# Kernel optimization log

Hardware: AMD Instinct MI355X
Metric: run time of the kernel (lower is better)

Reference implementation:

```python
import jax, jax.numpy as jnp
import numpy as np

KERN = 2  # matches init kwarg


def _avgpool(x):
    # non-overlapping avg pool kernel=stride=KERN on (N,C,H,W)
    N, C, H, W = x.shape
    return x.reshape(N, C, H // KERN, KERN, W // KERN, KERN).mean(axis=(3, 5))


def _pair_sum(mu1, var1, mu2, var2):
    # mu*, var*: (N, D). Broadcast to (N, N, D) and reduce to scalar.
    d = mu1[:, None, :] - mu2[None, :, :]
    s = var1[:, None, :] + var2[None, :, :]
    return jnp.sum(jnp.exp(-0.5 * (d * d / s + jnp.log(s))))


def setup_inputs() -> dict:
    key = jax.random.key(0)
    k1, k2, k3, k4 = jax.random.split(key, 4)
    shp = (128, 16, 32, 32)
    return {
        "mu_a": jax.random.normal(k1, shp, dtype=jnp.float32),
        "logvar_a": jax.random.normal(k2, shp, dtype=jnp.float32),
        "mu_b": jax.random.normal(k3, shp, dtype=jnp.float32),
        "logvar_b": jax.random.normal(k4, shp, dtype=jnp.float32),
    }


def reference(mu_a, logvar_a, mu_b, logvar_b):
    inv_k2 = 1.0 / (KERN * KERN)
    ma = _avgpool(mu_a)
    mb = _avgpool(mu_b)
    va = _avgpool(jnp.exp(logvar_a)) * inv_k2
    vb = _avgpool(jnp.exp(logvar_b)) * inv_k2
    N = ma.shape[0]
    ma, mb = ma.reshape(N, -1), mb.reshape(N, -1)
    va, vb = va.reshape(N, -1), vb.reshape(N, -1)
    vaa = _pair_sum(ma, va, ma, va)
    vab = _pair_sum(ma, va, mb, vb)
    vbb = _pair_sum(mb, vb, mb, vb)
    return vaa + vbb - 2.0 * vab
```

## Files before the change

kernel.cpp:

```cpp
#include <hip/hip_runtime.h>

#define NN 128
#define CC_ 16
#define HH 32
#define WW 32
#define DD 4096
#define ND (NN*DD)

#define MU_SCALE 0.8493218002880191f

__global__ __launch_bounds__(256) void pool_kernel(
    const float* __restrict__ mu_a, const float* __restrict__ lv_a,
    const float* __restrict__ mu_b, const float* __restrict__ lv_b,
    float* __restrict__ ws, float* __restrict__ out)
{
    int t = blockIdx.x * 256 + threadIdx.x;
    if (t == 0) out[0] = 0.0f;

    int wo = t & 15;
    int ho = (t >> 4) & 15;
    int c  = (t >> 8) & 15;
    int n  = t >> 12;

    int base = ((n * CC_ + c) * HH + 2 * ho) * WW + 2 * wo;

    float2 a0 = *(const float2*)(mu_a + base);
    float2 a1 = *(const float2*)(mu_a + base + WW);
    float2 la0 = *(const float2*)(lv_a + base);
    float2 la1 = *(const float2*)(lv_a + base + WW);
    float2 b0 = *(const float2*)(mu_b + base);
    float2 b1 = *(const float2*)(mu_b + base + WW);
    float2 lb0 = *(const float2*)(lv_b + base);
    float2 lb1 = *(const float2*)(lv_b + base + WW);

    const float ms = 0.25f * MU_SCALE;
    float ma_v = ms * (a0.x + a0.y + a1.x + a1.y);
    float mb_v = ms * (b0.x + b0.y + b1.x + b1.y);
    float va_v = 0.0625f * (__expf(la0.x) + __expf(la0.y) + __expf(la1.x) + __expf(la1.y));
    float vb_v = 0.0625f * (__expf(lb0.x) + __expf(lb0.y) + __expf(lb1.x) + __expf(lb1.y));

    ws[t]          = ma_v;
    ws[ND + t]     = va_v;
    ws[2 * ND + t] = mb_v;
    ws[3 * ND + t] = vb_v;
}

#define JCHUNK 32

__global__ __launch_bounds__(256) void pair_kernel(
    const float* __restrict__ ws, float* __restrict__ out)
{
    const float* __restrict__ ma = ws;
    const float* __restrict__ va = ws + ND;
    const float* __restrict__ mb = ws + 2 * ND;
    const float* __restrict__ vb = ws + 3 * ND;

    const int d  = blockIdx.x * 256 + threadIdx.x;
    const int i0 = (blockIdx.y >> 2) * 4;
    const int j0 = (blockIdx.y & 3) * JCHUNK;

    float rma[4], rva[4], rmb[4], rvb[4];
#pragma unroll
    for (int k = 0; k < 4; ++k) {
        rma[k] = ma[(i0 + k) * DD + d];
        rva[k] = va[(i0 + k) * DD + d];
        rmb[k] = mb[(i0 + k) * DD + d];
        rvb[k] = vb[(i0 + k) * DD + d];
    }

    float acc_aa = 0.0f, acc_bb = 0.0f, acc_ab = 0.0f;

    for (int j = j0; j < j0 + JCHUNK; ++j) {
        float jma = ma[j * DD + d];
        float jva = va[j * DD + d];
        float jmb = mb[j * DD + d];
        float jvb = vb[j * DD + d];
#pragma unroll
        for (int k = 0; k < 4; ++k) {
            {
                float dd = rma[k] - jma;
                float s  = rva[k] + jva;
                float r  = __builtin_amdgcn_rsqf(s);
                float q  = dd * r;
                float e  = __builtin_amdgcn_exp2f(-(q * q));
                acc_aa = fmaf(e, r, acc_aa);
            }
            {
                float dd = rmb[k] - jmb;
                float s  = rvb[k] + jvb;
                float r  = __builtin_amdgcn_rsqf(s);
                float q  = dd * r;
                float e  = __builtin_amdgcn_exp2f(-(q * q));
                acc_bb = fmaf(e, r, acc_bb);
            }
            {
                float dd = rma[k] - jmb;
                float s  = rva[k] + jvb;
                float r  = __builtin_amdgcn_rsqf(s);
                float q  = dd * r;
                float e  = __builtin_amdgcn_exp2f(-(q * q));
                acc_ab = fmaf(e, r, acc_ab);
            }
        }
    }

    float part = acc_aa + acc_bb - 2.0f * acc_ab;

#pragma unroll
    for (int off = 32; off > 0; off >>= 1)
        part += __shfl_down(part, off, 64);

    __shared__ float wsum[4];
    int lane = threadIdx.x & 63;
    int wv   = threadIdx.x >> 6;
    if (lane == 0) wsum[wv] = part;
    __syncthreads();
    if (threadIdx.x == 0) {
        float s = wsum[0] + wsum[1] + wsum[2] + wsum[3];
        atomicAdd(out, s);
    }
}

extern "C" void kernel_launch(void* const* d_in, const int* in_sizes, int n_in,
                              void* d_out, int out_size, void* d_ws, size_t ws_size,
                              hipStream_t stream) {
    const float* mu_a = (const float*)d_in[0];
    const float* lv_a = (const float*)d_in[1];
    const float* mu_b = (const float*)d_in[2];
    const float* lv_b = (const float*)d_in[3];
    float* out = (float*)d_out;
    float* ws  = (float*)d_ws;

    pool_kernel<<<dim3(ND / 256), 256, 0, stream>>>(mu_a, lv_a, mu_b, lv_b, ws, out);
    pair_kernel<<<dim3(DD / 256, (NN / 4) * (NN / JCHUNK)), 256, 0, stream>>>(ws, out);
}
```

Baseline: 134.0 us.

## Interleave pooled a/b buffers and use packed float2 math in pair kernel

The pool kernel now writes the a and b means as one float2 array and the a and b variances as another, so the pair kernel issues two 8-byte loads per j instead of four 4-byte loads. The pair kernel arithmetic moves to 2-wide vector types, meant to map subtract, add, multiply and fma onto packed FP32 instructions, and the j loop is unrolled by 2. rsq and exp2 stay scalar, and since the transcendentals likely bound the kernel, the gain may be limited.

After: 123.8 us. -7.6%, faster.

```diff
diff --git a/kernel.cpp b/kernel.cpp
--- a/kernel.cpp
+++ b/kernel.cpp
@@ -7,12 +7,14 @@
 #define DD 4096
 #define ND (NN*DD)
 
+typedef float v2f __attribute__((ext_vector_type(2)));
+
 #define MU_SCALE 0.8493218002880191f
 
 __global__ __launch_bounds__(256) void pool_kernel(
     const float* __restrict__ mu_a, const float* __restrict__ lv_a,
     const float* __restrict__ mu_b, const float* __restrict__ lv_b,
-    float* __restrict__ ws, float* __restrict__ out)
+    float2* __restrict__ wm, float2* __restrict__ wv, float* __restrict__ out)
 {
     int t = blockIdx.x * 256 + threadIdx.x;
     if (t == 0) out[0] = 0.0f;
@@ -39,72 +41,71 @@
     float va_v = 0.0625f * (__expf(la0.x) + __expf(la0.y) + __expf(la1.x) + __expf(la1.y));
     float vb_v = 0.0625f * (__expf(lb0.x) + __expf(lb0.y) + __expf(lb1.x) + __expf(lb1.y));
 
-    ws[t]          = ma_v;
-    ws[ND + t]     = va_v;
-    ws[2 * ND + t] = mb_v;
-    ws[3 * ND + t] = vb_v;
+    wm[t] = make_float2(ma_v, mb_v);
+    wv[t] = make_float2(va_v, vb_v);
 }
 
 #define JCHUNK 32
 
+__device__ __forceinline__ void pair_group(
+    v2f& acc, v2f mi, v2f mj, v2f vi, v2f vj)
+{
+    v2f dd = mi - mj;
+    v2f s  = vi + vj;
+    v2f r;
+    r.x = __builtin_amdgcn_rsqf(s.x);
+    r.y = __builtin_amdgcn_rsqf(s.y);
+    v2f q  = dd * r;
+    v2f qq = q * q;
+    v2f e;
+    e.x = __builtin_amdgcn_exp2f(-qq.x);
+    e.y = __builtin_amdgcn_exp2f(-qq.y);
+    acc += e * r;
+}
+
 __global__ __launch_bounds__(256) void pair_kernel(
-    const float* __restrict__ ws, float* __restrict__ out)
+    const float2* __restrict__ wm, const float2* __restrict__ wv,
+    float* __restrict__ out)
 {
-    const float* __restrict__ ma = ws;
-    const float* __restrict__ va = ws + ND;
-    const float* __restrict__ mb = ws + 2 * ND;
-    const float* __restrict__ vb = ws + 3 * ND;
-
     const int d  = blockIdx.x * 256 + threadIdx.x;
     const int i0 = (blockIdx.y >> 2) * 4;
     const int j0 = (blockIdx.y & 3) * JCHUNK;
 
-    float rma[4], rva[4], rmb[4], rvb[4];
+    v2f pma[2], pmb[2], pva[2], pvb[2];
 #pragma unroll
-    for (int k = 0; k < 4; ++k) {
-        rma[k] = ma[(i0 + k) * DD + d];
-        rva[k] = va[(i0 + k) * DD + d];
-        rmb[k] = mb[(i0 + k) * DD + d];
-        rvb[k] = vb[(i0 + k) * DD + d];
+    for (int p = 0; p < 2; ++p) {
+        float2 m0 = wm[(i0 + 2 * p) * DD + d];
+        float2 m1 = wm[(i0 + 2 * p + 1) * DD + d];
+        float2 v0 = wv[(i0 + 2 * p) * DD + d];
+        float2 v1 = wv[(i0 + 2 * p + 1) * DD + d];
+        pma[p] = (v2f){m0.x, m1.x};
+        pmb[p] = (v2f){m0.y, m1.y};
+        pva[p] = (v2f){v0.x, v1.x};
+        pvb[p] = (v2f){v0.y, v1.y};
     }
 
-    float acc_aa = 0.0f, acc_bb = 0.0f, acc_ab = 0.0f;
+    v2f acc_aa = (v2f){0.0f, 0.0f};
+    v2f acc_bb = (v2f){0.0f, 0.0f};
+    v2f acc_ab = (v2f){0.0f, 0.0f};
 
+#pragma unroll 2
     for (int j = j0; j < j0 + JCHUNK; ++j) {
-        float jma = ma[j * DD + d];
-        float jva = va[j * DD + d];
-        float jmb = mb[j * DD + d];
-        float jvb = vb[j * DD + d];
+        float2 jm = wm[j * DD + d];
+        float2 jv = wv[j * DD + d];
+        v2f jma2 = (v2f){jm.x, jm.x};
+        v2f jmb2 = (v2f){jm.y, jm.y};
+        v2f jva2 = (v2f){jv.x, jv.x};
+        v2f jvb2 = (v2f){jv.y, jv.y};
 #pragma unroll
-        for (int k = 0; k < 4; ++k) {
-            {
-                float dd = rma[k] - jma;
-                float s  = rva[k] + jva;
-                float r  = __builtin_amdgcn_rsqf(s);
-                float q  = dd * r;
-                float e  = __builtin_amdgcn_exp2f(-(q * q));
-                acc_aa = fmaf(e, r, acc_aa);
-            }
-            {
-                float dd = rmb[k] - jmb;
-                float s  = rvb[k] + jvb;
-                float r  = __builtin_amdgcn_rsqf(s);
-                float q  = dd * r;
-                float e  = __builtin_amdgcn_exp2f(-(q * q));
-                acc_bb = fmaf(e, r, acc_bb);
-            }
-            {
-                float dd = rma[k] - jmb;
-                float s  = rva[k] + jvb;
-                float r  = __builtin_amdgcn_rsqf(s);
-                float q  = dd * r;
-                float e  = __builtin_amdgcn_exp2f(-(q * q));
-                acc_ab = fmaf(e, r, acc_ab);
-            }
+        for (int p = 0; p < 2; ++p) {
+            pair_group(acc_aa, pma[p], jma2, pva[p], jva2);
+            pair_group(acc_bb, pmb[p], jmb2, pvb[p], jvb2);
+            pair_group(acc_ab, pma[p], jmb2, pva[p], jvb2);
         }
     }
 
-    float part = acc_aa + acc_bb - 2.0f * acc_ab;
+    float part = (acc_aa.x + acc_aa.y) + (acc_bb.x + acc_bb.y)
+               - 2.0f * (acc_ab.x + acc_ab.y);
 
 #pragma unroll
     for (int off = 32; off > 0; off >>= 1)
@@ -112,8 +113,8 @@
 
     __shared__ float wsum[4];
     int lane = threadIdx.x & 63;
-    int wv   = threadIdx.x >> 6;
-    if (lane == 0) wsum[wv] = part;
+    int wv_  = threadIdx.x >> 6;
+    if (lane == 0) wsum[wv_] = part;
     __syncthreads();
     if (threadIdx.x == 0) {
         float s = wsum[0] + wsum[1] + wsum[2] + wsum[3];
@@ -129,8 +130,9 @@
     const float* mu_b = (const float*)d_in[2];
     const float* lv_b = (const float*)d_in[3];
     float* out = (float*)d_out;
-    float* ws  = (float*)d_ws;
+    float2* wm = (float2*)d_ws;
+    float2* wv = ((float2*)d_ws) + ND;
 
-    pool_kernel<<<dim3(ND / 256), 256, 0, stream>>>(mu_a, lv_a, mu_b, lv_b, ws, out);
-    pair_kernel<<<dim3(DD / 256, (NN / 4) * (NN / JCHUNK)), 256, 0, stream>>>(ws, out);
+    pool_kernel<<<dim3(ND / 256), 256, 0, stream>>>(mu_a, lv_a, mu_b, lv_b, wm, wv, out);
+    pair_kernel<<<dim3(DD / 256, (NN / 4) * (NN / JCHUNK)), 256, 0, stream>>>(wm, wv, out);
 }
```
